# Kernel tuning notes

Hardware: AMD Instinct MI355X
Metric: run time of the kernel (lower is better)

The kernel has to match this reference:

```python
import jax, jax.numpy as jnp
import numpy as np

V, BLK, L, H, C, FF = 50257, 2048, 6, 8, 512, 2048
D = C // H  # head_dim = 64

def setup_inputs() -> dict:
    key = jax.random.key(0)
    ks = jax.random.split(key, 16)
    s = 0.02
    proj_std = 0.02 / np.sqrt(2 * L)
    return {
        'idx': jax.random.randint(ks[0], (2, 2048), 0, V, dtype=jnp.int64),
        'wte': jax.random.normal(ks[1], (V, C), jnp.float32) * s,
        'wpe': jax.random.normal(ks[2], (BLK, C), jnp.float32) * s,
        'ln1_w': jnp.ones((L, C), jnp.float32), 'ln1_b': jnp.zeros((L, C), jnp.float32),
        'c_attn_w': jax.random.normal(ks[3], (L, 3 * C, C), jnp.float32) * s,
        'c_proj_w': jax.random.normal(ks[4], (L, C, C), jnp.float32) * proj_std,
        'ln2_w': jnp.ones((L, C), jnp.float32), 'ln2_b': jnp.zeros((L, C), jnp.float32),
        'fc_w': jax.random.normal(ks[5], (L, FF, C), jnp.float32) * s,
        'proj_w': jax.random.normal(ks[6], (L, C, FF), jnp.float32) * proj_std,
        'lnf_w': jnp.ones((C,), jnp.float32), 'lnf_b': jnp.zeros((C,), jnp.float32),
    }

def _layernorm(x, w, b, eps=1e-5):
    mu = jnp.mean(x, axis=-1, keepdims=True)
    var = jnp.var(x, axis=-1, keepdims=True)
    return (x - mu) * jax.lax.rsqrt(var + eps) * w + b

def _attn(x, attn_w, proj_w, mask):
    B, T, _ = x.shape
    qkv = jnp.einsum('btc,fc->btf', x, attn_w)  # (B,T,3C)
    q, k, v = jnp.split(qkv, 3, axis=-1)
    q = q.reshape(B, T, H, D)
    k = k.reshape(B, T, H, D)
    v = v.reshape(B, T, H, D)
    scale = 1.0 / np.sqrt(D)
    att = jnp.einsum('bthd,bshd->bhts', q, k) * scale  # (B,H,T,T)
    att = jnp.where(mask, att, -jnp.inf)
    att = jax.nn.softmax(att, axis=-1)
    y = jnp.einsum('bhts,bshd->bthd', att, v).reshape(B, T, C)
    return jnp.einsum('btc,oc->bto', y, proj_w)

def reference(idx, wte, wpe, ln1_w, ln1_b, c_attn_w, c_proj_w, ln2_w, ln2_b, fc_w, proj_w, lnf_w, lnf_b):
    B, T = idx.shape
    pos = jnp.arange(T)
    x = wte[idx] + wpe[pos]  # (B,T,C); dropout p=0
    mask = jnp.tril(jnp.ones((T, T), bool))[None, None]
    for i in range(L):
        x = x + _attn(_layernorm(x, ln1_w[i], ln1_b[i]), c_attn_w[i], c_proj_w[i], mask)
        h = _layernorm(x, ln2_w[i], ln2_b[i])
        h = jax.nn.gelu(jnp.einsum('btc,fc->btf', h, fc_w[i]), approximate=False)
        x = x + jnp.einsum('btf,cf->btc', h, proj_w[i])
    x = _layernorm(x, lnf_w, lnf_b)
    logits = jnp.einsum('btc,vc->btv', x, wte)  # tied lm_head
    return logits
```

## Files before the change

kernel.cpp:

```cpp
#include <hip/hip_runtime.h>

typedef unsigned short u16;
typedef short bf16x8 __attribute__((ext_vector_type(8)));
typedef float f32x4 __attribute__((ext_vector_type(4)));
typedef unsigned short u16x4 __attribute__((ext_vector_type(4)));
typedef unsigned short u16x8 __attribute__((ext_vector_type(8)));
typedef unsigned int u32x2 __attribute__((ext_vector_type(2)));

#define B_ 2
#define T_ 2048
#define C_ 512
#define H_ 8
#define FF_ 2048
#define L_ 6
#define V_ 50257
#define M_ (B_*T_)

__device__ __forceinline__ u16 f2b(float f) {
  union { float f; unsigned u; } v; v.f = f;
  unsigned r = v.u + 0x7FFFu + ((v.u >> 16) & 1u);
  return (u16)(r >> 16);
}
__device__ __forceinline__ float b2f(u16 u) {
  union { unsigned u; float f; } v; v.u = ((unsigned)u) << 16; return v.f;
}
__device__ __forceinline__ unsigned pk_bf16(float lo, float hi) {
  unsigned r;
  asm volatile("v_cvt_pk_bf16_f32 %0, %1, %2" : "=v"(r) : "v"(lo), "v"(hi));
  return r;
}

__device__ __forceinline__ void async16(const void* g, void* l) {
  __builtin_amdgcn_global_load_lds((const __attribute__((address_space(1))) unsigned int*)g,
                                   (__attribute__((address_space(3))) unsigned int*)l, 16, 0, 0);
}

__device__ __forceinline__ bf16x8 scale8(u16x8 v, float s) {
  union { bf16x8 b; unsigned u[4]; } r;
#pragma unroll
  for (int i = 0; i < 4; i++)
    r.u[i] = pk_bf16(b2f(v[2*i]) * s, b2f(v[2*i+1]) * s);
  return r.b;
}

__global__ void cvt_bf16_k(const f32x4* __restrict__ src, u16x4* __restrict__ dst, int n4) {
  int i = blockIdx.x * blockDim.x + threadIdx.x;
  int stride = gridDim.x * blockDim.x;
  for (; i < n4; i += stride) {
    f32x4 v = src[i];
    u16x4 o;
    o[0] = f2b(v[0]); o[1] = f2b(v[1]); o[2] = f2b(v[2]); o[3] = f2b(v[3]);
    dst[i] = o;
  }
}

__global__ void embed_k(const int* __restrict__ idx, const float* __restrict__ wte,
                        const float* __restrict__ wpe, float* __restrict__ x) {
  int t = blockIdx.x * 256 + threadIdx.x;
  int row = t >> 7;
  int c4 = t & 127;
  int tok = idx[row];
  int pos = row & (T_ - 1);
  f32x4 a = ((const f32x4*)(wte + (long)tok * C_))[c4];
  f32x4 p = ((const f32x4*)(wpe + (long)pos * C_))[c4];
  ((f32x4*)x)[t] = a + p;
}

__global__ void ln_k(const float* __restrict__ x, const float* __restrict__ w,
                     const float* __restrict__ b, u16* __restrict__ out) {
  int wv = threadIdx.x >> 6;
  int lane = threadIdx.x & 63;
  int row = blockIdx.x * 4 + wv;
  const f32x4* xr = (const f32x4*)(x + (long)row * C_);
  f32x4 v0 = xr[lane * 2], v1 = xr[lane * 2 + 1];
  float s = 0.f, s2 = 0.f;
#pragma unroll
  for (int j = 0; j < 4; j++) { s += v0[j] + v1[j]; s2 += v0[j]*v0[j] + v1[j]*v1[j]; }
#pragma unroll
  for (int off = 32; off >= 1; off >>= 1) { s += __shfl_xor(s, off); s2 += __shfl_xor(s2, off); }
  float mu = s * (1.f / C_);
  float inv = rsqrtf(s2 * (1.f / C_) - mu * mu + 1e-5f);
  const f32x4* wr = (const f32x4*)w;
  const f32x4* br = (const f32x4*)b;
  f32x4 w0 = wr[lane*2], w1 = wr[lane*2+1], b0 = br[lane*2], b1 = br[lane*2+1];
  u16x8 o;
#pragma unroll
  for (int j = 0; j < 4; j++) {
    o[j]     = f2b((v0[j] - mu) * inv * w0[j] + b0[j]);
    o[j + 4] = f2b((v1[j] - mu) * inv * w1[j] + b1[j]);
  }
  *(u16x8*)(out + (long)row * C_ + lane * 8) = o;
}

template<int EPI, int BM>
__global__ __launch_bounds__(256) void gemm_bt_k(
    const u16* __restrict__ A, const u16* __restrict__ Bw,
    u16* __restrict__ Cb, float* __restrict__ Cf,
    int N, int K, int ldc)
{
  constexpr int MT = BM / 32;
  __shared__ __align__(16) u16 sA[2][BM * 32];
  __shared__ __align__(16) u16 sB[2][128 * 32];
  const int tid = threadIdx.x;
  const int n0 = blockIdx.x * 128;
  const int m0 = blockIdx.y * BM;
  const int w = tid >> 6;
  const int lane = tid & 63;
  const int wm = (w >> 1) * (BM / 2);
  const int wn = (w & 1) * 64;
  const int g = lane >> 4;
  const int l15 = lane & 15;

  f32x4 acc[MT][4] = {};

  const int nk = K >> 5;
  int arow0 = tid >> 2, ak0 = (tid & 3) * 8;
  int c1 = tid + 256;
  int arow1 = c1 >> 2, ak1 = (c1 & 3) * 8;
  int brow0 = n0 + arow0; if (brow0 > N - 1) brow0 = N - 1;
  int brow1 = n0 + arow1; if (brow1 > N - 1) brow1 = N - 1;
  const u16* gA0 = A + (long)(m0 + arow0) * K + ak0;
  const u16* gA1 = A + (long)(m0 + arow1) * K + ak1;
  const u16* gB0 = Bw + (long)brow0 * K + ak0;
  const u16* gB1 = Bw + (long)brow1 * K + ak1;
  const int lb0 = (w * 64) * 8;
  const int lb1 = (256 + w * 64) * 8;

  auto stage = [&](int buf, int kt) {
    int ko = kt << 5;
    async16(gA0 + ko, &sA[buf][lb0]);
    if constexpr (BM == 128) async16(gA1 + ko, &sA[buf][lb1]);
    async16(gB0 + ko, &sB[buf][lb0]);
    async16(gB1 + ko, &sB[buf][lb1]);
  };

  stage(0, 0);
  __syncthreads();
  int cur = 0;
  for (int kt = 0; kt < nk; kt++) {
    if (kt + 1 < nk) stage(cur ^ 1, kt + 1);
    const u16* pa = sA[cur];
    const u16* pb = sB[cur];
    bf16x8 af[MT], bfr[4];
#pragma unroll
    for (int mt = 0; mt < MT; mt++)
      af[mt] = *(const bf16x8*)(pa + (wm + mt * 16 + l15) * 32 + g * 8);
#pragma unroll
    for (int nt = 0; nt < 4; nt++)
      bfr[nt] = *(const bf16x8*)(pb + (wn + nt * 16 + l15) * 32 + g * 8);
#pragma unroll
    for (int mt = 0; mt < MT; mt++)
#pragma unroll
      for (int nt = 0; nt < 4; nt++)
        acc[mt][nt] = __builtin_amdgcn_mfma_f32_16x16x32_bf16(af[mt], bfr[nt], acc[mt][nt], 0, 0, 0);
    __syncthreads();
    cur ^= 1;
  }

#pragma unroll
  for (int mt = 0; mt < MT; mt++) {
    int m = m0 + wm + mt * 16 + g * 4;
#pragma unroll
    for (int nt = 0; nt < 4; nt++) {
      int n = n0 + wn + nt * 16 + l15;
      f32x4 v = acc[mt][nt];
#pragma unroll
      for (int r = 0; r < 4; r++) {
        long ci = (long)(m + r) * ldc + n;
        if (EPI == 0) {
          Cb[ci] = f2b(v[r]);
        } else if (EPI == 1) {
          Cf[ci] += v[r];
        } else if (EPI == 2) {
          float f = v[r];
          f = 0.5f * f * (1.0f + erff(f * 0.70710678118654752f));
          Cb[ci] = f2b(f);
        } else {
          if (n < N) Cf[ci] = v[r];
        }
      }
    }
  }
}

__global__ __launch_bounds__(128) void attn_k(const u16* __restrict__ qkv, u16* __restrict__ out) {
  const int bh = blockIdx.y;
  const int b = bh >> 3;
  const int h = bh & 7;
  const int tid = threadIdx.x;
  const int wv = tid >> 6;
  const int lane = tid & 63;
  const int g = lane >> 4;
  const int l15 = lane & 15;
  const int qA = blockIdx.x >> 1;
  const int halfsel = blockIdx.x & 1;

  __shared__ __align__(16) u16 Ks[2][64 * 64];
  __shared__ __align__(16) u16 Vt[2][64 * 72];
  __shared__ __align__(16) u16 Ps[2][16 * 64];

  const long base = (long)b * T_ * 1536;
  const u16* kbase = qkv + base + 512 + h * 64;
  const u16* vbase = qkv + base + 1024 + h * 64;
  const int kq = tid & 15;
  const int dg = tid >> 4;
  const float qscale = 0.18033688011112042f;

  for (int ph = 0; ph < 2; ph++) {
    const int qblk = (ph == 0) ? qA : 31 - qA;
    const int q0 = qblk * 64 + halfsel * 32 + wv * 16;

    const u16* qrow = qkv + base + (long)(q0 + l15) * 1536 + h * 64;
    bf16x8 qf0 = scale8(*(const u16x8*)(qrow + g * 8), qscale);
    bf16x8 qf1 = scale8(*(const u16x8*)(qrow + 32 + g * 8), qscale);

    f32x4 o[4] = {};
    float mrun[4] = {-1e30f, -1e30f, -1e30f, -1e30f};
    float lrun[4] = {0.f, 0.f, 0.f, 0.f};
    const int kvend = qblk * 64 + 64;

    u16x8 vreg[4];
#pragma unroll
    for (int i = 0; i < 4; i++) {
      int chunk = i * 128 + tid;
      int row = chunk >> 3, c8 = chunk & 7;
      async16(kbase + (long)row * 1536 + (c8 ^ (row & 7)) * 8,
              &Ks[0][(i * 128 + wv * 64) * 8]);
    }
#pragma unroll
    for (int t = 0; t < 4; t++)
      vreg[t] = *(const u16x8*)(vbase + (long)(kq + 16 * t) * 1536 + dg * 8);
#pragma unroll
    for (int e = 0; e < 8; e++) {
      int d = dg * 8 + e;
      u32x2 wq = { (unsigned)vreg[0][e] | ((unsigned)vreg[1][e] << 16),
                   (unsigned)vreg[2][e] | ((unsigned)vreg[3][e] << 16) };
      *(u32x2*)(&Vt[0][d * 72 + kq * 4]) = wq;
    }
    __syncthreads();

    int cur = 0;
    for (int j0 = 0; j0 < kvend; j0 += 64, cur ^= 1) {
      const bool more = (j0 + 64) < kvend;
      if (more) {
        int jn = j0 + 64;
#pragma unroll
        for (int i = 0; i < 4; i++) {
          int chunk = i * 128 + tid;
          int row = chunk >> 3, c8 = chunk & 7;
          async16(kbase + (long)(jn + row) * 1536 + (c8 ^ (row & 7)) * 8,
                  &Ks[cur ^ 1][(i * 128 + wv * 64) * 8]);
        }
#pragma unroll
        for (int t = 0; t < 4; t++)
          vreg[t] = *(const u16x8*)(vbase + (long)(jn + kq + 16 * t) * 1536 + dg * 8);
      }

      f32x4 s[4] = {};
      const u16* kp = Ks[cur];
#pragma unroll
      for (int t = 0; t < 4; t++) {
        int row = t * 16 + l15;
        const u16* kr = kp + row * 64;
        bf16x8 k0 = *(const bf16x8*)(kr + ((g ^ (row & 7)) * 8));
        bf16x8 k1 = *(const bf16x8*)(kr + (((4 + g) ^ (row & 7)) * 8));
        s[t] = __builtin_amdgcn_mfma_f32_16x16x32_bf16(qf0, k0, s[t], 0, 0, 0);
        s[t] = __builtin_amdgcn_mfma_f32_16x16x32_bf16(qf1, k1, s[t], 0, 0, 0);
      }

      const bool diag = (j0 + 64) == kvend;
      u16* pw = Ps[wv];
#pragma unroll
      for (int r = 0; r < 4; r++) {
        int row = q0 + g * 4 + r;
        float v0 = s[0][r], v1 = s[1][r], v2 = s[2][r], v3 = s[3][r];
        if (diag) {
          if (j0 +      l15 > row) v0 = -1e30f;
          if (j0 + 16 + l15 > row) v1 = -1e30f;
          if (j0 + 32 + l15 > row) v2 = -1e30f;
          if (j0 + 48 + l15 > row) v3 = -1e30f;
        }
        float mloc = fmaxf(fmaxf(v0, v1), fmaxf(v2, v3));
        float m = mrun[r];
        if (!__all(mloc <= m + 8.0f)) {
          float mx = mloc;
          mx = fmaxf(mx, __shfl_xor(mx, 1));
          mx = fmaxf(mx, __shfl_xor(mx, 2));
          mx = fmaxf(mx, __shfl_xor(mx, 4));
          mx = fmaxf(mx, __shfl_xor(mx, 8));
          float mn = fmaxf(m, mx);
          float sc2 = exp2f(m - mn);
          lrun[r] *= sc2;
#pragma unroll
          for (int dt = 0; dt < 4; dt++) o[dt][r] *= sc2;
          m = mn; mrun[r] = mn;
        }
        float e0 = exp2f(v0 - m), e1 = exp2f(v1 - m);
        float e2 = exp2f(v2 - m), e3 = exp2f(v3 - m);
        lrun[r] += (e0 + e1) + (e2 + e3);
        u32x2 pkq = { pk_bf16(e0, e1), pk_bf16(e2, e3) };
        int prow = g * 4 + r;
        int byt = prow * 128 + ((((l15 >> 1) ^ (prow & 7)) << 4)) + (l15 & 1) * 8;
        *(u32x2*)((char*)pw + byt) = pkq;
      }

      const u16* vt = Vt[cur];
      bf16x8 pf0 = *(const bf16x8*)((char*)pw + l15 * 128 + (((g) ^ (l15 & 7)) << 4));
      bf16x8 pf1 = *(const bf16x8*)((char*)pw + l15 * 128 + (((4 + g) ^ (l15 & 7)) << 4));
#pragma unroll
      for (int dt = 0; dt < 4; dt++) {
        int d = dt * 16 + l15;
        bf16x8 vf0 = *(const bf16x8*)(vt + d * 72 + g * 8);
        bf16x8 vf1 = *(const bf16x8*)(vt + d * 72 + 32 + g * 8);
        o[dt] = __builtin_amdgcn_mfma_f32_16x16x32_bf16(pf0, vf0, o[dt], 0, 0, 0);
        o[dt] = __builtin_amdgcn_mfma_f32_16x16x32_bf16(pf1, vf1, o[dt], 0, 0, 0);
      }

      if (more) {
#pragma unroll
        for (int e = 0; e < 8; e++) {
          int d = dg * 8 + e;
          u32x2 wq = { (unsigned)vreg[0][e] | ((unsigned)vreg[1][e] << 16),
                       (unsigned)vreg[2][e] | ((unsigned)vreg[3][e] << 16) };
          *(u32x2*)(&Vt[cur ^ 1][d * 72 + kq * 4]) = wq;
        }
      }
      __syncthreads();
    }

#pragma unroll
    for (int r = 0; r < 4; r++) {
      float ls = lrun[r];
      ls += __shfl_xor(ls, 1); ls += __shfl_xor(ls, 2);
      ls += __shfl_xor(ls, 4); ls += __shfl_xor(ls, 8);
      float inv = 1.0f / ls;
      int row = q0 + g * 4 + r;
      u16* orow = out + (long)(b * T_ + row) * C_ + h * 64;
#pragma unroll
      for (int dt = 0; dt < 4; dt++)
        orow[dt * 16 + l15] = f2b(o[dt][r] * inv);
    }
  }
}

extern "C" void kernel_launch(void* const* d_in, const int* in_sizes, int n_in,
                              void* d_out, int out_size, void* d_ws, size_t ws_size,
                              hipStream_t stream) {
  const int*   idx    = (const int*)  d_in[0];
  const float* wte    = (const float*)d_in[1];
  const float* wpe    = (const float*)d_in[2];
  const float* ln1w   = (const float*)d_in[3];
  const float* ln1b   = (const float*)d_in[4];
  const float* wattn  = (const float*)d_in[5];
  const float* wcproj = (const float*)d_in[6];
  const float* ln2w   = (const float*)d_in[7];
  const float* ln2b   = (const float*)d_in[8];
  const float* wfc    = (const float*)d_in[9];
  const float* wproj2 = (const float*)d_in[10];
  const float* lnfw   = (const float*)d_in[11];
  const float* lnfb   = (const float*)d_in[12];
  float* out = (float*)d_out;

  char* p = (char*)d_ws;
  size_t off = 0;
  auto alloc = [&](size_t bytes) -> void* {
    void* r = p + off; off += (bytes + 255) & ~(size_t)255; return r;
  };
  float* x    = (float*)alloc((size_t)M_ * C_ * 4);
  u16* xn     = (u16*)alloc((size_t)M_ * C_ * 2);
  u16* qkvb   = (u16*)alloc((size_t)M_ * 3 * C_ * 2);
  u16* attb   = (u16*)alloc((size_t)M_ * C_ * 2);
  u16* hb     = (u16*)alloc((size_t)M_ * FF_ * 2);
  u16* wteB   = (u16*)alloc((size_t)V_ * C_ * 2);
  u16* wattnB = (u16*)alloc((size_t)L_ * 3 * C_ * C_ * 2);
  u16* wprojB = (u16*)alloc((size_t)L_ * C_ * C_ * 2);
  u16* wfcB   = (u16*)alloc((size_t)L_ * FF_ * C_ * 2);
  u16* wp2B   = (u16*)alloc((size_t)L_ * C_ * FF_ * 2);
  if (off > ws_size) return;

  auto cvt = [&](const float* s, u16* d, long n) {
    int n4 = (int)(n >> 2);
    int blocks = (n4 + 255) / 256; if (blocks > 4096) blocks = 4096;
    cvt_bf16_k<<<dim3(blocks), dim3(256), 0, stream>>>((const f32x4*)s, (u16x4*)d, n4);
  };
  cvt(wte, wteB, (long)V_ * C_);
  cvt(wattn, wattnB, (long)L_ * 3 * C_ * C_);
  cvt(wcproj, wprojB, (long)L_ * C_ * C_);
  cvt(wfc, wfcB, (long)L_ * FF_ * C_);
  cvt(wproj2, wp2B, (long)L_ * C_ * FF_);

  embed_k<<<dim3(M_ * C_ / 4 / 256), dim3(256), 0, stream>>>(idx, wte, wpe, x);

  for (int l = 0; l < L_; l++) {
    ln_k<<<dim3(M_ / 4), dim3(256), 0, stream>>>(x, ln1w + l * C_, ln1b + l * C_, xn);
    gemm_bt_k<0, 64><<<dim3(12, 64), dim3(256), 0, stream>>>(
        xn, wattnB + (size_t)l * 3 * C_ * C_, qkvb, nullptr, 3 * C_, C_, 3 * C_);
    attn_k<<<dim3(32, B_ * H_), dim3(128), 0, stream>>>(qkvb, attb);
    gemm_bt_k<1, 64><<<dim3(4, 64), dim3(256), 0, stream>>>(
        attb, wprojB + (size_t)l * C_ * C_, nullptr, x, C_, C_, C_);
    ln_k<<<dim3(M_ / 4), dim3(256), 0, stream>>>(x, ln2w + l * C_, ln2b + l * C_, xn);
    gemm_bt_k<2, 128><<<dim3(16, 32), dim3(256), 0, stream>>>(
        xn, wfcB + (size_t)l * FF_ * C_, hb, nullptr, FF_, C_, FF_);
    gemm_bt_k<1, 64><<<dim3(4, 64), dim3(256), 0, stream>>>(
        hb, wp2B + (size_t)l * C_ * FF_, nullptr, x, C_, FF_, C_);
  }
  ln_k<<<dim3(M_ / 4), dim3(256), 0, stream>>>(x, lnfw, lnfb, xn);
  gemm_bt_k<3, 128><<<dim3((V_ + 127) / 128, 32), dim3(256), 0, stream>>>(
      xn, wteB, nullptr, out, V_, C_, V_);
}
```

Before: 1.505 ms.

## Add dedicated 256x128 LM-head GEMM with XCD swizzle; split attention blocks per q-tile

Adds a dedicated LM-head GEMM kernel with 512 threads and 256x128 tiles. It uses a 1D grid whose block index is swizzled across the 8 chiplets so that neighbouring tiles share the weight and activation tiles in L2. The aim is to cut global traffic and improve reuse for the largest GEMM (4096x50257x512). Separately, the attention kernel no longer processes a balanced pair of q-blocks per workgroup; each workgroup handles one q-tile and the grid is doubled to 64, with the heaviest tiles launched first. This raises parallelism but relies on the scheduler to balance the causal workload, and the new 1D grid swizzle assumes its block count divides evenly by 8.

```diff
diff --git a/kernel.cpp b/kernel.cpp
--- a/kernel.cpp
+++ b/kernel.cpp
@@ -171,13 +171,91 @@
           Cb[ci] = f2b(v[r]);
         } else if (EPI == 1) {
           Cf[ci] += v[r];
-        } else if (EPI == 2) {
+        } else {
           float f = v[r];
           f = 0.5f * f * (1.0f + erff(f * 0.70710678118654752f));
           Cb[ci] = f2b(f);
-        } else {
-          if (n < N) Cf[ci] = v[r];
         }
+      }
+    }
+  }
+}
+
+__global__ __launch_bounds__(512) void gemm_lmhead_k(
+    const u16* __restrict__ A, const u16* __restrict__ Bw,
+    float* __restrict__ Cf, int N)
+{
+  __shared__ __align__(16) u16 sA[2][256 * 32];
+  __shared__ __align__(16) u16 sB[2][128 * 32];
+  const int K = 512;
+  const int nwg = gridDim.x;
+  const int cpx = nwg >> 3;
+  const int bid = blockIdx.x;
+  const int swz = (bid & 7) * cpx + (bid >> 3);
+  const int ntiles = (N + 127) >> 7;
+  const int n0 = (swz % ntiles) * 128;
+  const int m0 = (swz / ntiles) * 256;
+  const int tid = threadIdx.x;
+  const int w = tid >> 6;
+  const int lane = tid & 63;
+  const int wm = (w >> 1) * 64;
+  const int wn = (w & 1) * 64;
+  const int g = lane >> 4;
+  const int l15 = lane & 15;
+
+  f32x4 acc[4][4] = {};
+
+  const int ac1 = tid + 512;
+  const u16* gA0 = A + (long)(m0 + (tid >> 2)) * K + (tid & 3) * 8;
+  const u16* gA1 = A + (long)(m0 + (ac1 >> 2)) * K + (ac1 & 3) * 8;
+  int brow = n0 + (tid >> 2); if (brow > N - 1) brow = N - 1;
+  const u16* gB0 = Bw + (long)brow * K + (tid & 3) * 8;
+  const int lbA0 = (w * 64) * 8;
+  const int lbA1 = (512 + w * 64) * 8;
+  const int lbB0 = (w * 64) * 8;
+
+  auto stage = [&](int buf, int kt) {
+    int ko = kt << 5;
+    async16(gA0 + ko, &sA[buf][lbA0]);
+    async16(gA1 + ko, &sA[buf][lbA1]);
+    async16(gB0 + ko, &sB[buf][lbB0]);
+  };
+
+  stage(0, 0);
+  __syncthreads();
+  int cur = 0;
+  const int nk = K >> 5;
+  for (int kt = 0; kt < nk; kt++) {
+    if (kt + 1 < nk) stage(cur ^ 1, kt + 1);
+    const u16* pa = sA[cur];
+    const u16* pb = sB[cur];
+    bf16x8 af[4], bfr[4];
+#pragma unroll
+    for (int mt = 0; mt < 4; mt++)
+      af[mt] = *(const bf16x8*)(pa + (wm + mt * 16 + l15) * 32 + g * 8);
+#pragma unroll
+    for (int nt = 0; nt < 4; nt++)
+      bfr[nt] = *(const bf16x8*)(pb + (wn + nt * 16 + l15) * 32 + g * 8);
+#pragma unroll
+    for (int mt = 0; mt < 4; mt++)
+#pragma unroll
+      for (int nt = 0; nt < 4; nt++)
+        acc[mt][nt] = __builtin_amdgcn_mfma_f32_16x16x32_bf16(af[mt], bfr[nt], acc[mt][nt], 0, 0, 0);
+    __syncthreads();
+    cur ^= 1;
+  }
+
+#pragma unroll
+  for (int mt = 0; mt < 4; mt++) {
+    int m = m0 + wm + mt * 16 + g * 4;
+#pragma unroll
+    for (int nt = 0; nt < 4; nt++) {
+      int n = n0 + wn + nt * 16 + l15;
+      f32x4 v = acc[mt][nt];
+      if (n < N) {
+#pragma unroll
+        for (int r = 0; r < 4; r++)
+          Cf[(long)(m + r) * N + n] = v[r];
       }
     }
   }
@@ -192,7 +270,7 @@
   const int lane = tid & 63;
   const int g = lane >> 4;
   const int l15 = lane & 15;
-  const int qA = blockIdx.x >> 1;
+  const int qblk = 31 - (blockIdx.x >> 1);
   const int halfsel = blockIdx.x & 1;
 
   __shared__ __align__(16) u16 Ks[2][64 * 64];
@@ -206,140 +284,137 @@
   const int dg = tid >> 4;
   const float qscale = 0.18033688011112042f;
 
-  for (int ph = 0; ph < 2; ph++) {
-    const int qblk = (ph == 0) ? qA : 31 - qA;
-    const int q0 = qblk * 64 + halfsel * 32 + wv * 16;
-
-    const u16* qrow = qkv + base + (long)(q0 + l15) * 1536 + h * 64;
-    bf16x8 qf0 = scale8(*(const u16x8*)(qrow + g * 8), qscale);
-    bf16x8 qf1 = scale8(*(const u16x8*)(qrow + 32 + g * 8), qscale);
-
-    f32x4 o[4] = {};
-    float mrun[4] = {-1e30f, -1e30f, -1e30f, -1e30f};
-    float lrun[4] = {0.f, 0.f, 0.f, 0.f};
-    const int kvend = qblk * 64 + 64;
-
-    u16x8 vreg[4];
-#pragma unroll
-    for (int i = 0; i < 4; i++) {
-      int chunk = i * 128 + tid;
-      int row = chunk >> 3, c8 = chunk & 7;
-      async16(kbase + (long)row * 1536 + (c8 ^ (row & 7)) * 8,
-              &Ks[0][(i * 128 + wv * 64) * 8]);
-    }
-#pragma unroll
-    for (int t = 0; t < 4; t++)
-      vreg[t] = *(const u16x8*)(vbase + (long)(kq + 16 * t) * 1536 + dg * 8);
-#pragma unroll
-    for (int e = 0; e < 8; e++) {
-      int d = dg * 8 + e;
-      u32x2 wq = { (unsigned)vreg[0][e] | ((unsigned)vreg[1][e] << 16),
-                   (unsigned)vreg[2][e] | ((unsigned)vreg[3][e] << 16) };
-      *(u32x2*)(&Vt[0][d * 72 + kq * 4]) = wq;
+  const int q0 = qblk * 64 + halfsel * 32 + wv * 16;
+
+  const u16* qrow = qkv + base + (long)(q0 + l15) * 1536 + h * 64;
+  bf16x8 qf0 = scale8(*(const u16x8*)(qrow + g * 8), qscale);
+  bf16x8 qf1 = scale8(*(const u16x8*)(qrow + 32 + g * 8), qscale);
+
+  f32x4 o[4] = {};
+  float mrun[4] = {-1e30f, -1e30f, -1e30f, -1e30f};
+  float lrun[4] = {0.f, 0.f, 0.f, 0.f};
+  const int kvend = qblk * 64 + 64;
+
+  u16x8 vreg[4];
+#pragma unroll
+  for (int i = 0; i < 4; i++) {
+    int chunk = i * 128 + tid;
+    int row = chunk >> 3, c8 = chunk & 7;
+    async16(kbase + (long)row * 1536 + (c8 ^ (row & 7)) * 8,
+            &Ks[0][(i * 128 + wv * 64) * 8]);
+  }
+#pragma unroll
+  for (int t = 0; t < 4; t++)
+    vreg[t] = *(const u16x8*)(vbase + (long)(kq + 16 * t) * 1536 + dg * 8);
+#pragma unroll
+  for (int e = 0; e < 8; e++) {
+    int d = dg * 8 + e;
+    u32x2 wq = { (unsigned)vreg[0][e] | ((unsigned)vreg[1][e] << 16),
+                 (unsigned)vreg[2][e] | ((unsigned)vreg[3][e] << 16) };
+    *(u32x2*)(&Vt[0][d * 72 + kq * 4]) = wq;
+  }
+  __syncthreads();
+
+  int cur = 0;
+  for (int j0 = 0; j0 < kvend; j0 += 64, cur ^= 1) {
+    const bool more = (j0 + 64) < kvend;
+    if (more) {
+      int jn = j0 + 64;
+#pragma unroll
+      for (int i = 0; i < 4; i++) {
+        int chunk = i * 128 + tid;
+        int row = chunk >> 3, c8 = chunk & 7;
+        async16(kbase + (long)(jn + row) * 1536 + (c8 ^ (row & 7)) * 8,
+                &Ks[cur ^ 1][(i * 128 + wv * 64) * 8]);
+      }
+#pragma unroll
+      for (int t = 0; t < 4; t++)
+        vreg[t] = *(const u16x8*)(vbase + (long)(jn + kq + 16 * t) * 1536 + dg * 8);
+    }
+
+    f32x4 s[4] = {};
+    const u16* kp = Ks[cur];
+#pragma unroll
+    for (int t = 0; t < 4; t++) {
+      int row = t * 16 + l15;
+      const u16* kr = kp + row * 64;
+      bf16x8 k0 = *(const bf16x8*)(kr + ((g ^ (row & 7)) * 8));
+      bf16x8 k1 = *(const bf16x8*)(kr + (((4 + g) ^ (row & 7)) * 8));
+      s[t] = __builtin_amdgcn_mfma_f32_16x16x32_bf16(qf0, k0, s[t], 0, 0, 0);
+      s[t] = __builtin_amdgcn_mfma_f32_16x16x32_bf16(qf1, k1, s[t], 0, 0, 0);
+    }
+
+    const bool diag = (j0 + 64) == kvend;
+    u16* pw = Ps[wv];
+#pragma unroll
+    for (int r = 0; r < 4; r++) {
+      int row = q0 + g * 4 + r;
+      float v0 = s[0][r], v1 = s[1][r], v2 = s[2][r], v3 = s[3][r];
+      if (diag) {
+        if (j0 +      l15 > row) v0 = -1e30f;
+        if (j0 + 16 + l15 > row) v1 = -1e30f;
+        if (j0 + 32 + l15 > row) v2 = -1e30f;
+        if (j0 + 48 + l15 > row) v3 = -1e30f;
+      }
+      float mloc = fmaxf(fmaxf(v0, v1), fmaxf(v2, v3));
+      float m = mrun[r];
+      if (!__all(mloc <= m + 8.0f)) {
+        float mx = mloc;
+        mx = fmaxf(mx, __shfl_xor(mx, 1));
+        mx = fmaxf(mx, __shfl_xor(mx, 2));
+        mx = fmaxf(mx, __shfl_xor(mx, 4));
+        mx = fmaxf(mx, __shfl_xor(mx, 8));
+        float mn = fmaxf(m, mx);
+        float sc2 = exp2f(m - mn);
+        lrun[r] *= sc2;
+#pragma unroll
+        for (int dt = 0; dt < 4; dt++) o[dt][r] *= sc2;
+        m = mn; mrun[r] = mn;
+      }
+      float e0 = exp2f(v0 - m), e1 = exp2f(v1 - m);
+      float e2 = exp2f(v2 - m), e3 = exp2f(v3 - m);
+      lrun[r] += (e0 + e1) + (e2 + e3);
+      u32x2 pkq = { pk_bf16(e0, e1), pk_bf16(e2, e3) };
+      int prow = g * 4 + r;
+      int byt = prow * 128 + ((((l15 >> 1) ^ (prow & 7)) << 4)) + (l15 & 1) * 8;
+      *(u32x2*)((char*)pw + byt) = pkq;
+    }
+
+    const u16* vt = Vt[cur];
+    bf16x8 pf0 = *(const bf16x8*)((char*)pw + l15 * 128 + (((g) ^ (l15 & 7)) << 4));
+    bf16x8 pf1 = *(const bf16x8*)((char*)pw + l15 * 128 + (((4 + g) ^ (l15 & 7)) << 4));
+#pragma unroll
+    for (int dt = 0; dt < 4; dt++) {
+      int d = dt * 16 + l15;
+      bf16x8 vf0 = *(const bf16x8*)(vt + d * 72 + g * 8);
+      bf16x8 vf1 = *(const bf16x8*)(vt + d * 72 + 32 + g * 8);
+      o[dt] = __builtin_amdgcn_mfma_f32_16x16x32_bf16(pf0, vf0, o[dt], 0, 0, 0);
+      o[dt] = __builtin_amdgcn_mfma_f32_16x16x32_bf16(pf1, vf1, o[dt], 0, 0, 0);
+    }
+
+    if (more) {
+#pragma unroll
+      for (int e = 0; e < 8; e++) {
+        int d = dg * 8 + e;
+        u32x2 wq = { (unsigned)vreg[0][e] | ((unsigned)vreg[1][e] << 16),
+                     (unsigned)vreg[2][e] | ((unsigned)vreg[3][e] << 16) };
+        *(u32x2*)(&Vt[cur ^ 1][d * 72 + kq * 4]) = wq;
+      }
     }
     __syncthreads();
-
-    int cur = 0;
-    for (int j0 = 0; j0 < kvend; j0 += 64, cur ^= 1) {
-      const bool more = (j0 + 64) < kvend;
-      if (more) {
-        int jn = j0 + 64;
-#pragma unroll
-        for (int i = 0; i < 4; i++) {
-          int chunk = i * 128 + tid;
-          int row = chunk >> 3, c8 = chunk & 7;
-          async16(kbase + (long)(jn + row) * 1536 + (c8 ^ (row & 7)) * 8,
-                  &Ks[cur ^ 1][(i * 128 + wv * 64) * 8]);
-        }
-#pragma unroll
-        for (int t = 0; t < 4; t++)
-          vreg[t] = *(const u16x8*)(vbase + (long)(jn + kq + 16 * t) * 1536 + dg * 8);
-      }
-
-      f32x4 s[4] = {};
-      const u16* kp = Ks[cur];
-#pragma unroll
-      for (int t = 0; t < 4; t++) {
-        int row = t * 16 + l15;
-        const u16* kr = kp + row * 64;
-        bf16x8 k0 = *(const bf16x8*)(kr + ((g ^ (row & 7)) * 8));
-        bf16x8 k1 = *(const bf16x8*)(kr + (((4 + g) ^ (row & 7)) * 8));
-        s[t] = __builtin_amdgcn_mfma_f32_16x16x32_bf16(qf0, k0, s[t], 0, 0, 0);
-        s[t] = __builtin_amdgcn_mfma_f32_16x16x32_bf16(qf1, k1, s[t], 0, 0, 0);
-      }
-
-      const bool diag = (j0 + 64) == kvend;
-      u16* pw = Ps[wv];
-#pragma unroll
-      for (int r = 0; r < 4; r++) {
-        int row = q0 + g * 4 + r;
-        float v0 = s[0][r], v1 = s[1][r], v2 = s[2][r], v3 = s[3][r];
-        if (diag) {
-          if (j0 +      l15 > row) v0 = -1e30f;
-          if (j0 + 16 + l15 > row) v1 = -1e30f;
-          if (j0 + 32 + l15 > row) v2 = -1e30f;
-          if (j0 + 48 + l15 > row) v3 = -1e30f;
-        }
-        float mloc = fmaxf(fmaxf(v0, v1), fmaxf(v2, v3));
-        float m = mrun[r];
-        if (!__all(mloc <= m + 8.0f)) {
-          float mx = mloc;
-          mx = fmaxf(mx, __shfl_xor(mx, 1));
-          mx = fmaxf(mx, __shfl_xor(mx, 2));
-          mx = fmaxf(mx, __shfl_xor(mx, 4));
-          mx = fmaxf(mx, __shfl_xor(mx, 8));
-          float mn = fmaxf(m, mx);
-          float sc2 = exp2f(m - mn);
-          lrun[r] *= sc2;
-#pragma unroll
-          for (int dt = 0; dt < 4; dt++) o[dt][r] *= sc2;
-          m = mn; mrun[r] = mn;
-        }
-        float e0 = exp2f(v0 - m), e1 = exp2f(v1 - m);
-        float e2 = exp2f(v2 - m), e3 = exp2f(v3 - m);
-        lrun[r] += (e0 + e1) + (e2 + e3);
-        u32x2 pkq = { pk_bf16(e0, e1), pk_bf16(e2, e3) };
-        int prow = g * 4 + r;
-        int byt = prow * 128 + ((((l15 >> 1) ^ (prow & 7)) << 4)) + (l15 & 1) * 8;
-        *(u32x2*)((char*)pw + byt) = pkq;
-      }
-
-      const u16* vt = Vt[cur];
-      bf16x8 pf0 = *(const bf16x8*)((char*)pw + l15 * 128 + (((g) ^ (l15 & 7)) << 4));
-      bf16x8 pf1 = *(const bf16x8*)((char*)pw + l15 * 128 + (((4 + g) ^ (l15 & 7)) << 4));
-#pragma unroll
-      for (int dt = 0; dt < 4; dt++) {
-        int d = dt * 16 + l15;
-        bf16x8 vf0 = *(const bf16x8*)(vt + d * 72 + g * 8);
-        bf16x8 vf1 = *(const bf16x8*)(vt + d * 72 + 32 + g * 8);
-        o[dt] = __builtin_amdgcn_mfma_f32_16x16x32_bf16(pf0, vf0, o[dt], 0, 0, 0);
-        o[dt] = __builtin_amdgcn_mfma_f32_16x16x32_bf16(pf1, vf1, o[dt], 0, 0, 0);
-      }
-
-      if (more) {
-#pragma unroll
-        for (int e = 0; e < 8; e++) {
-          int d = dg * 8 + e;
-          u32x2 wq = { (unsigned)vreg[0][e] | ((unsigned)vreg[1][e] << 16),
-                       (unsigned)vreg[2][e] | ((unsigned)vreg[3][e] << 16) };
-          *(u32x2*)(&Vt[cur ^ 1][d * 72 + kq * 4]) = wq;
-        }
-      }
-      __syncthreads();
-    }
-
-#pragma unroll
-    for (int r = 0; r < 4; r++) {
-      float ls = lrun[r];
-      ls += __shfl_xor(ls, 1); ls += __shfl_xor(ls, 2);
-      ls += __shfl_xor(ls, 4); ls += __shfl_xor(ls, 8);
-      float inv = 1.0f / ls;
-      int row = q0 + g * 4 + r;
-      u16* orow = out + (long)(b * T_ + row) * C_ + h * 64;
-#pragma unroll
-      for (int dt = 0; dt < 4; dt++)
-        orow[dt * 16 + l15] = f2b(o[dt][r] * inv);
-    }
+  }
+
+#pragma unroll
+  for (int r = 0; r < 4; r++) {
+    float ls = lrun[r];
+    ls += __shfl_xor(ls, 1); ls += __shfl_xor(ls, 2);
+    ls += __shfl_xor(ls, 4); ls += __shfl_xor(ls, 8);
+    float inv = 1.0f / ls;
+    int row = q0 + g * 4 + r;
+    u16* orow = out + (long)(b * T_ + row) * C_ + h * 64;
+#pragma unroll
+    for (int dt = 0; dt < 4; dt++)
+      orow[dt * 16 + l15] = f2b(o[dt][r] * inv);
   }
 }
 
@@ -395,7 +470,7 @@
     ln_k<<<dim3(M_ / 4), dim3(256), 0, stream>>>(x, ln1w + l * C_, ln1b + l * C_, xn);
     gemm_bt_k<0, 64><<<dim3(12, 64), dim3(256), 0, stream>>>(
         xn, wattnB + (size_t)l * 3 * C_ * C_, qkvb, nullptr, 3 * C_, C_, 3 * C_);
-    attn_k<<<dim3(32, B_ * H_), dim3(128), 0, stream>>>(qkvb, attb);
+    attn_k<<<dim3(64, B_ * H_), dim3(128), 0, stream>>>(qkvb, attb);
     gemm_bt_k<1, 64><<<dim3(4, 64), dim3(256), 0, stream>>>(
         attb, wprojB + (size_t)l * C_ * C_, nullptr, x, C_, C_, C_);
     ln_k<<<dim3(M_ / 4), dim3(256), 0, stream>>>(x, ln2w + l * C_, ln2b + l * C_, xn);
@@ -405,6 +480,6 @@
         hb, wp2B + (size_t)l * C_ * FF_, nullptr, x, C_, FF_, C_);
   }
   ln_k<<<dim3(M_ / 4), dim3(256), 0, stream>>>(x, lnfw, lnfb, xn);
-  gemm_bt_k<3, 128><<<dim3((V_ + 127) / 128, 32), dim3(256), 0, stream>>>(
-      xn, wteB, nullptr, out, V_, C_, V_);
-}
+  gemm_lmhead_k<<<dim3(((V_ + 127) / 128) * (M_ / 256)), dim3(512), 0, stream>>>(
+      xn, wteB, out, V_);
+}
```

After: 1.422 ms. -5.5%, faster.
